# Performance work log

Measured on AMD Instinct MI355X. Metric: run time of the kernel, lower is better.

The kernel has to match this reference:

```python
import jax, jax.numpy as jnp
import numpy as np

B, T, C = 8, 1024, 1024
H, HS = 16, 64            # n_head, head_size
K, STRIDE = 32, 16        # block_length, stride_length
WIN = 128                 # local_window_size
EPS = 1e-5


def _ln(z, w):
    m = jnp.mean(z, axis=-1, keepdims=True)
    v = jnp.var(z, axis=-1, keepdims=True)
    return (z - m) / jnp.sqrt(v + EPS) * w


def setup_inputs() -> dict:
    key = jax.random.key(0)
    ks = jax.random.split(key, 8)
    s = 0.02
    return {
        "x": jax.random.normal(ks[0], (B, T, C), jnp.float32),
        "c_attn_w": jax.random.normal(ks[1], (3 * C, C), jnp.float32) * s,
        "conv_w": jax.random.normal(ks[2], (HS, HS, K), jnp.float32) * s,
        "ln_comp_w": jnp.ones((HS,), jnp.float32),
        "ln_local_w": jnp.ones((C,), jnp.float32),
        "gate_w1": jax.random.normal(ks[3], (C, 2 * C), jnp.float32) * s,
        "gate_ln_w": jnp.ones((C,), jnp.float32),
        "gate_w2": jax.random.normal(ks[4], (2, C), jnp.float32) * s,
        "c_proj_w": jax.random.normal(ks[5], (C, C), jnp.float32) * s,
    }


def reference(x, c_attn_w, conv_w, ln_comp_w, ln_local_w, gate_w1, gate_ln_w, gate_w2, c_proj_w):
    qkv = jnp.einsum('btc,oc->bto', x, c_attn_w)          # [B,T,3C]
    q, k, v = jnp.split(qkv, 3, axis=-1)
    def heads(t):
        return t.reshape(B, T, H, HS).transpose(0, 2, 1, 3)  # [B,H,T,hs]
    q, k, v = heads(q), heads(k), heads(v)

    # CompressionMLP: Conv1d over time + LayerNorm(hs) + exact GELU
    def compress(t):
        xr = t.transpose(0, 1, 3, 2).reshape(B * H, HS, T)   # [B*H, hs, T]
        co = jax.lax.conv_general_dilated(
            xr, conv_w, window_strides=(STRIDE,), padding='VALID',
            dimension_numbers=('NCH', 'OIH', 'NCH'))          # [B*H, hs, NB]
        co = co.transpose(0, 2, 1)                            # [B*H, NB, hs]
        co = jax.nn.gelu(_ln(co, ln_comp_w), approximate=False)
        nb = co.shape[1]
        return co.reshape(B, H, nb, HS)

    kc = compress(k)
    vc = compress(v)
    NB = kc.shape[2]  # 63
    scale = 1.0 / np.sqrt(HS)

    ti = jnp.arange(T)
    band = (ti[None, :] <= ti[:, None]) & (ti[None, :] >= ti[:, None] - WIN)  # [T,T]
    s_loc = jnp.einsum('bhqd,bhkd->bhqk', q, k) * scale
    s_loc = jnp.where(band[None, None], s_loc, -jnp.inf)
    local_out = jnp.einsum('bhqk,bhkd->bhqd', jax.nn.softmax(s_loc, axis=-1), v)
    local_out = local_out.transpose(0, 2, 1, 3).reshape(B, T, C)
    local_norm = _ln(local_out, ln_local_w)

    # compressed-KV attention with block-causal mask: block j <= token i
    bj = jnp.arange(NB)
    cmask = bj[None, :] <= ti[:, None]                        # [T,NB]
    s_cmp = jnp.einsum('bhqd,bhkd->bhqk', q, kc) * scale
    s_cmp = jnp.where(cmask[None, None], s_cmp, -jnp.inf)
    comp_out = jnp.einsum('bhqk,bhkd->bhqd', jax.nn.softmax(s_cmp, axis=-1), vc)
    comp_out = comp_out.transpose(0, 2, 1, 3).reshape(B, T, C)

    # AttentionGating: last-token features -> Linear -> LN -> ReLU -> Linear -> softmax
    feats = jnp.concatenate([local_norm[:, -1, :], comp_out[:, -1, :]], axis=-1)  # [B,2C]
    h = jax.nn.relu(_ln(feats @ gate_w1.T, gate_ln_w))
    gates = jax.nn.softmax(h @ gate_w2.T, axis=-1)            # [B,2]

    combined = gates[:, None, 0:1] * local_norm + gates[:, None, 1:2] * comp_out
    y = jnp.einsum('btc,oc->bto', combined, c_proj_w)
    return y
```

## Files before the change

### kernel.cpp

```cpp
#include <hip/hip_runtime.h>
#include <cstdint>
#include <cmath>
#include <cstddef>

typedef unsigned int u32;
typedef unsigned short u16;
typedef __bf16 bf16x8 __attribute__((ext_vector_type(8)));
typedef float f32x4 __attribute__((ext_vector_type(4)));
typedef u32 u32x4 __attribute__((ext_vector_type(4)));
typedef u32 u32x2 __attribute__((ext_vector_type(2)));

#define DEV static __device__ __forceinline__

DEV float bflo(u32 u) { return __uint_as_float(u << 16); }
DEV float bfhi(u32 u) { return __uint_as_float(u & 0xffff0000u); }
DEV u16 f2bf(float f) {
  u32 u = __float_as_uint(f);
  u += 0x7fffu + ((u >> 16) & 1u);
  return (u16)(u >> 16);
}
DEV f32x4 unpack_bf4(u32x2 r) {
  return (f32x4){bflo(r[0]), bfhi(r[0]), bflo(r[1]), bfhi(r[1])};
}
DEV float wredsum(float v) {
#pragma unroll
  for (int o = 32; o; o >>= 1) v += __shfl_xor(v, o, 64);
  return v;
}

DEV void gload_lds16(const u16* g, u16* lds_base) {
  __builtin_amdgcn_global_load_lds((const __attribute__((address_space(1))) void*)g,
                                   (__attribute__((address_space(3))) void*)lds_base,
                                   16, 0, 0);
}

__global__ __launch_bounds__(256) void fused_cast(const float* __restrict__ x,
                                                  const float* __restrict__ aw,
                                                  const float* __restrict__ pw,
                                                  const float* __restrict__ cw,
                                                  u16* __restrict__ xb,
                                                  u16* __restrict__ wab,
                                                  u16* __restrict__ wpb,
                                                  u16* __restrict__ wcb,
                                                  u16* __restrict__ kcb,
                                                  u16* __restrict__ vcb) {
  const int blk = blockIdx.x;
  if (blk < 12288) {
    const float* src;
    u16* dst;
    int base;
    if (blk < 8192) { src = x; dst = xb; base = blk; }
    else if (blk < 11264) { src = aw; dst = wab; base = blk - 8192; }
    else { src = pw; dst = wpb; base = blk - 11264; }
    const size_t idx = ((size_t)base * 256 + threadIdx.x) * 4;
    const f32x4 v = *(const f32x4*)&src[idx];
    u32x2 r;
    r[0] = (u32)f2bf(v[0]) | ((u32)f2bf(v[1]) << 16);
    r[1] = (u32)f2bf(v[2]) | ((u32)f2bf(v[3]) << 16);
    *(u32x2*)&dst[idx] = r;
  } else if (blk < 12800) {
    const int idx = (blk - 12288) * 256 + threadIdx.x;
    const int o = idx >> 11;
    const int rest = idx & 2047;
    const int i = rest >> 5;
    const int kk = rest & 31;
    wcb[(o << 11) + (kk << 6) + i] = f2bf(cw[idx]);
  } else {
    for (int i = threadIdx.x; i < 8192; i += 256) {
      const int bh = i >> 6, d = i & 63;
      kcb[bh * 4096 + 63 * 64 + d] = 0;
      vcb[bh * 4096 + d * 64 + 63] = 0;
    }
  }
}

template <int OUT_BF16>
__global__ __launch_bounds__(256, 4) void gemm_bt(const u16* __restrict__ A,
                                                  const u16* __restrict__ Bm,
                                                  void* __restrict__ out,
                                                  int M, int N, int K) {
  __shared__ u16 As[128 * 32];
  __shared__ u16 Bs[128 * 32];
  const int tid = threadIdx.x;
  const int lane = tid & 63;
  const int w = tid >> 6;
  const int row0 = blockIdx.x * 128;
  const int col0 = blockIdx.y * 128;
  const int wm = (w >> 1) * 64, wn = (w & 1) * 64;
  const int lr = lane & 15, lq = lane >> 4;
  const int srow = lane >> 2;
  const int scol = (lane & 3) * 8;

  f32x4 acc[4][4] = {};

  for (int k0 = 0; k0 < K; k0 += 32) {
    __syncthreads();
#pragma unroll
    for (int p = 0; p < 2; ++p) {
      const int base_r = p * 64 + w * 16;
      gload_lds16(&A[(size_t)(row0 + base_r + srow) * K + k0 + scol], &As[base_r * 32]);
      gload_lds16(&Bm[(size_t)(col0 + base_r + srow) * K + k0 + scol], &Bs[base_r * 32]);
    }
    __syncthreads();
    bf16x8 af[4], bfr[4];
#pragma unroll
    for (int i = 0; i < 4; ++i) {
      af[i] = *(const bf16x8*)&As[(wm + i * 16 + lr) * 32 + lq * 8];
      bfr[i] = *(const bf16x8*)&Bs[(wn + i * 16 + lr) * 32 + lq * 8];
    }
#pragma unroll
    for (int i = 0; i < 4; ++i)
#pragma unroll
      for (int j = 0; j < 4; ++j)
        acc[i][j] = __builtin_amdgcn_mfma_f32_16x16x32_bf16(af[i], bfr[j], acc[i][j], 0, 0, 0);
  }
#pragma unroll
  for (int i = 0; i < 4; ++i)
#pragma unroll
    for (int j = 0; j < 4; ++j)
#pragma unroll
      for (int rr = 0; rr < 4; ++rr) {
        const int gr = row0 + wm + i * 16 + lq * 4 + rr;
        const int gc = col0 + wn + j * 16 + lr;
        const float v = acc[i][j][rr];
        if (OUT_BF16)
          ((u16*)out)[(size_t)gr * N + gc] = f2bf(v);
        else
          ((float*)out)[(size_t)gr * N + gc] = v;
      }
}

__global__ __launch_bounds__(256) void compress_kernel(const u16* __restrict__ qkv,
                                                       const u16* __restrict__ Wc,
                                                       const float* __restrict__ ln_w,
                                                       u16* __restrict__ kcb,
                                                       u16* __restrict__ vcb) {
  __shared__ u16 As[2][64 * 32];
  __shared__ u16 Bs[2][64 * 32];
  __shared__ float Cs[64][65];
  const int tid = threadIdx.x;
  const int lane = tid & 63, w = tid >> 6;
  const int lr = lane & 15, lq = lane >> 4;
  const int r0 = blockIdx.x * 64;
  const int srcoff = 1024 + (int)blockIdx.y * 1024;

  const int arow = tid >> 2, acol = (tid & 3) * 8;
  const int gr = r0 + arow;
  const int bh = gr / 63;
  const int nb = gr - bh * 63;
  const int b = bh >> 4, h = bh & 15;
  const size_t abase = (size_t)(b * 1024 + nb * 16) * 3072 + srcoff + h * 64 + acol;
  const size_t bbase = (size_t)arow * 2048 + acol;

  f32x4 acc[4] = {};
  {
    gload_lds16(&qkv[abase], &As[0][w * 512]);
    gload_lds16(&Wc[bbase], &Bs[0][w * 512]);
  }
  for (int it = 0; it < 64; ++it) {
    const int cur = it & 1;
    __syncthreads();
    if (it < 63) {
      const int k0 = (it + 1) * 32;
      const int kk = k0 >> 6, i0 = k0 & 63;
      gload_lds16(&qkv[abase + (size_t)kk * 3072 + i0], &As[cur ^ 1][w * 512]);
      gload_lds16(&Wc[bbase + k0], &Bs[cur ^ 1][w * 512]);
    }
    const bf16x8 af = *(const bf16x8*)&As[cur][(w * 16 + lr) * 32 + lq * 8];
#pragma unroll
    for (int j = 0; j < 4; ++j) {
      const bf16x8 bfr = *(const bf16x8*)&Bs[cur][(j * 16 + lr) * 32 + lq * 8];
      acc[j] = __builtin_amdgcn_mfma_f32_16x16x32_bf16(af, bfr, acc[j], 0, 0, 0);
    }
  }
  __syncthreads();
#pragma unroll
  for (int j = 0; j < 4; ++j)
#pragma unroll
    for (int rr = 0; rr < 4; ++rr)
      Cs[w * 16 + lq * 4 + rr][j * 16 + lr] = acc[j][rr];
  __syncthreads();
  if (tid < 64) {
    const int gr2 = r0 + tid;
    const int bh2 = gr2 / 63;
    const int nb2 = gr2 - bh2 * 63;
    float s = 0.f, s2 = 0.f;
#pragma unroll 8
    for (int d = 0; d < 64; ++d) {
      const float xv = Cs[tid][d];
      s += xv;
      s2 += xv * xv;
    }
    const float m = s * (1.f / 64.f);
    const float inv = rsqrtf(s2 * (1.f / 64.f) - m * m + 1e-5f);
    if (blockIdx.y == 0) {
      const size_t gb = (size_t)bh2 * 4096 + nb2 * 64;
#pragma unroll 8
      for (int d = 0; d < 64; ++d) {
        const float z = (Cs[tid][d] - m) * inv * ln_w[d];
        kcb[gb + d] = f2bf(0.5f * z * (1.f + erff(z * 0.70710678118f)));
      }
    } else {
      const size_t gb = (size_t)bh2 * 4096 + nb2;
#pragma unroll 8
      for (int d = 0; d < 64; ++d) {
        const float z = (Cs[tid][d] - m) * inv * ln_w[d];
        vcb[gb + d * 64] = f2bf(0.5f * z * (1.f + erff(z * 0.70710678118f)));
      }
    }
  }
}

__global__ __launch_bounds__(256) void attn_fused(const u16* __restrict__ qkv,
                                                  const u16* __restrict__ kcb,
                                                  const u16* __restrict__ vcb,
                                                  u16* __restrict__ loc,
                                                  u16* __restrict__ outc) {
  __shared__ __align__(16) char smem[53248];
  u16* Ks = (u16*)smem;
  u16* Vt = (u16*)smem;
  u16* Ps = (u16*)(smem + 27648);
  const int bh = blockIdx.x;
  const int b = bh >> 4, h = bh & 15;
  const int i0 = blockIdx.y * 64;
  const int jbase = i0 - 128;
  const int tid = threadIdx.x;
  const int lane = tid & 63, w = tid >> 6;
  const int lr = lane & 15, lq = lane >> 4;

  u32x4 vreg[6];
#pragma unroll
  for (int c = 0; c < 6; ++c) {
    const int lin = c * 256 + tid;
    const int s = lin >> 3, d0 = (lin & 7) * 8;
    const int j = jbase + s;
    u32x4 kval = {0, 0, 0, 0}, vval = {0, 0, 0, 0};
    if (j >= 0) {
      const size_t ro = (size_t)(b * 1024 + j) * 3072 + h * 64 + d0;
      kval = *(const u32x4*)&qkv[ro + 1024];
      vval = *(const u32x4*)&qkv[ro + 2048];
    }
    vreg[c] = vval;
    *(u32x4*)&Ks[s * 72 + d0] = kval;
  }
  bf16x8 qf[2];
  {
    const size_t qrow = (size_t)(b * 1024 + i0 + w * 16 + lr) * 3072 + h * 64;
#pragma unroll
    for (int ks = 0; ks < 2; ++ks) qf[ks] = *(const bf16x8*)&qkv[qrow + ks * 32 + lq * 8];
  }
  __syncthreads();

  f32x4 sa[9];
#pragma unroll
  for (int j9 = 0; j9 < 9; ++j9) sa[j9] = (f32x4){0.f, 0.f, 0.f, 0.f};
#pragma unroll
  for (int ks = 0; ks < 2; ++ks)
#pragma unroll
    for (int j9 = 0; j9 < 9; ++j9) {
      const int jt = w + j9;
      const bf16x8 kf = *(const bf16x8*)&Ks[(jt * 16 + lr) * 72 + ks * 32 + lq * 8];
      sa[j9] = __builtin_amdgcn_mfma_f32_16x16x32_bf16(qf[ks], kf, sa[j9], 0, 0, 0);
    }

  const float NINF = -__builtin_inff();
  float mx[4] = {NINF, NINF, NINF, NINF};
#pragma unroll
  for (int j9 = 0; j9 < 9; ++j9) {
    const int s = (w + j9) * 16 + lr;
#pragma unroll
    for (int rr = 0; rr < 4; ++rr) {
      const int qi = w * 16 + lq * 4 + rr;
      const bool valid = (jbase + s >= 0) && (s >= qi) && (s <= qi + 128);
      const float v = valid ? sa[j9][rr] * 0.125f : NINF;
      sa[j9][rr] = v;
      mx[rr] = fmaxf(mx[rr], v);
    }
  }
#pragma unroll
  for (int rr = 0; rr < 4; ++rr)
#pragma unroll
    for (int o = 1; o < 16; o <<= 1) mx[rr] = fmaxf(mx[rr], __shfl_xor(mx[rr], o, 64));
  float sum[4] = {0.f, 0.f, 0.f, 0.f};
#pragma unroll
  for (int j9 = 0; j9 < 9; ++j9)
#pragma unroll
    for (int rr = 0; rr < 4; ++rr) {
      const float p = __expf(sa[j9][rr] - mx[rr]);
      sa[j9][rr] = p;
      sum[rr] += p;
    }
#pragma unroll
  for (int rr = 0; rr < 4; ++rr) {
#pragma unroll
    for (int o = 1; o < 16; o <<= 1) sum[rr] += __shfl_xor(sum[rr], o, 64);
    sum[rr] = 1.0f / sum[rr];
  }
  __syncthreads();

#pragma unroll
  for (int j9 = 0; j9 < 9; ++j9) {
    const int jt = w + j9;
#pragma unroll
    for (int rr = 0; rr < 4; ++rr)
      Ps[(w * 16 + lq * 4 + rr) * 200 + jt * 16 + lr] = f2bf(sa[j9][rr] * sum[rr]);
  }
  {
    const int jz = (w == 0) ? 9 : (w == 1) ? 0 : (w == 2) ? 11 : 2;
#pragma unroll
    for (int rr = 0; rr < 4; ++rr) Ps[(w * 16 + lq * 4 + rr) * 200 + jz * 16 + lr] = 0;
  }
#pragma unroll
  for (int c = 0; c < 6; ++c) {
    const int lin = c * 256 + tid;
    const int s = lin >> 3, d0 = (lin & 7) * 8;
    const u32x4 val = vreg[c];
#pragma unroll
    for (int q = 0; q < 4; ++q) {
      Vt[(d0 + 2 * q) * 200 + s] = (u16)(val[q] & 0xffffu);
      Vt[(d0 + 2 * q + 1) * 200 + s] = (u16)(val[q] >> 16);
    }
  }
  __syncthreads();

  const int W = (w >> 1) * 32;
  f32x4 oa[4];
#pragma unroll
  for (int jt = 0; jt < 4; ++jt) oa[jt] = (f32x4){0.f, 0.f, 0.f, 0.f};
#pragma unroll
  for (int ks = 0; ks < 5; ++ks) {
    const bf16x8 pf = *(const bf16x8*)&Ps[(w * 16 + lr) * 200 + W + ks * 32 + lq * 8];
#pragma unroll
    for (int jt = 0; jt < 4; ++jt) {
      const bf16x8 vf = *(const bf16x8*)&Vt[(jt * 16 + lr) * 200 + W + ks * 32 + lq * 8];
      oa[jt] = __builtin_amdgcn_mfma_f32_16x16x32_bf16(pf, vf, oa[jt], 0, 0, 0);
    }
  }
#pragma unroll
  for (int jt = 0; jt < 4; ++jt)
#pragma unroll
    for (int rr = 0; rr < 4; ++rr)
      loc[(size_t)(b * 1024 + i0 + w * 16 + lq * 4 + rr) * 1024 + h * 64 + jt * 16 + lr] =
          f2bf(oa[jt][rr]);

  __syncthreads();
  u16* Kc = (u16*)smem;
  u16* Vc = (u16*)(smem + 9216);
  u16* Pc = (u16*)(smem + 18432);
  const size_t cb = (size_t)bh * 4096;
  for (int c2 = tid; c2 < 512; c2 += 256) {
    const int nb = c2 >> 3, d0 = (c2 & 7) * 8;
    *(u32x4*)&Kc[nb * 72 + d0] = *(const u32x4*)&kcb[cb + nb * 64 + d0];
  }
  for (int c2 = tid; c2 < 512; c2 += 256) {
    const int d = c2 >> 3, n0 = (c2 & 7) * 8;
    *(u32x4*)&Vc[d * 72 + n0] = *(const u32x4*)&vcb[cb + d * 64 + n0];
  }
  __syncthreads();

  f32x4 ca[4];
#pragma unroll
  for (int j = 0; j < 4; ++j) ca[j] = (f32x4){0.f, 0.f, 0.f, 0.f};
#pragma unroll
  for (int ks = 0; ks < 2; ++ks)
#pragma unroll
    for (int j = 0; j < 4; ++j) {
      const bf16x8 kf = *(const bf16x8*)&Kc[(j * 16 + lr) * 72 + ks * 32 + lq * 8];
      ca[j] = __builtin_amdgcn_mfma_f32_16x16x32_bf16(qf[ks], kf, ca[j], 0, 0, 0);
    }
  float mc[4] = {NINF, NINF, NINF, NINF};
#pragma unroll
  for (int j = 0; j < 4; ++j) {
    const int s = j * 16 + lr;
#pragma unroll
    for (int rr = 0; rr < 4; ++rr) {
      const int i = i0 + w * 16 + lq * 4 + rr;
      const bool valid = (s <= i) && (s < 63);
      const float v = valid ? ca[j][rr] * 0.125f : NINF;
      ca[j][rr] = v;
      mc[rr] = fmaxf(mc[rr], v);
    }
  }
#pragma unroll
  for (int rr = 0; rr < 4; ++rr)
#pragma unroll
    for (int o = 1; o < 16; o <<= 1) mc[rr] = fmaxf(mc[rr], __shfl_xor(mc[rr], o, 64));
  float sc[4] = {0.f, 0.f, 0.f, 0.f};
#pragma unroll
  for (int j = 0; j < 4; ++j)
#pragma unroll
    for (int rr = 0; rr < 4; ++rr) {
      const float p = __expf(ca[j][rr] - mc[rr]);
      ca[j][rr] = p;
      sc[rr] += p;
    }
#pragma unroll
  for (int rr = 0; rr < 4; ++rr) {
#pragma unroll
    for (int o = 1; o < 16; o <<= 1) sc[rr] += __shfl_xor(sc[rr], o, 64);
    sc[rr] = 1.0f / sc[rr];
  }
#pragma unroll
  for (int j = 0; j < 4; ++j)
#pragma unroll
    for (int rr = 0; rr < 4; ++rr)
      Pc[(w * 16 + lq * 4 + rr) * 72 + j * 16 + lr] = f2bf(ca[j][rr] * sc[rr]);
  __syncthreads();

  f32x4 co[4];
#pragma unroll
  for (int jt = 0; jt < 4; ++jt) co[jt] = (f32x4){0.f, 0.f, 0.f, 0.f};
#pragma unroll
  for (int ks = 0; ks < 2; ++ks) {
    const bf16x8 pf = *(const bf16x8*)&Pc[(w * 16 + lr) * 72 + ks * 32 + lq * 8];
#pragma unroll
    for (int jt = 0; jt < 4; ++jt) {
      const bf16x8 vf = *(const bf16x8*)&Vc[(jt * 16 + lr) * 72 + ks * 32 + lq * 8];
      co[jt] = __builtin_amdgcn_mfma_f32_16x16x32_bf16(pf, vf, co[jt], 0, 0, 0);
    }
  }
#pragma unroll
  for (int jt = 0; jt < 4; ++jt)
#pragma unroll
    for (int rr = 0; rr < 4; ++rr)
      outc[(size_t)(b * 1024 + i0 + w * 16 + lq * 4 + rr) * 1024 + h * 64 + jt * 16 + lr] =
          f2bf(co[jt][rr]);
}

__global__ __launch_bounds__(256) void ln_feats(const u16* __restrict__ locb,
                                                const u16* __restrict__ compb,
                                                const float* __restrict__ lnw,
                                                float* __restrict__ feats) {
  const int b = blockIdx.x, tid = threadIdx.x;
  const size_t base = ((size_t)b * 1024 + 1023) * 1024 + tid * 4;
  const f32x4 v = unpack_bf4(*(const u32x2*)&locb[base]);
  float s = v[0] + v[1] + v[2] + v[3];
  float s2 = v[0] * v[0] + v[1] * v[1] + v[2] * v[2] + v[3] * v[3];
  s = wredsum(s);
  s2 = wredsum(s2);
  __shared__ float rs[4], rs2[4];
  const int w = tid >> 6, lane = tid & 63;
  if (!lane) { rs[w] = s; rs2[w] = s2; }
  __syncthreads();
  s = rs[0] + rs[1] + rs[2] + rs[3];
  s2 = rs2[0] + rs2[1] + rs2[2] + rs2[3];
  const float m = s * (1.f / 1024.f);
  const float inv = rsqrtf(s2 * (1.f / 1024.f) - m * m + 1e-5f);
  const f32x4 wv = *(const f32x4*)&lnw[tid * 4];
  f32x4 o;
#pragma unroll
  for (int k = 0; k < 4; ++k) o[k] = (v[k] - m) * inv * wv[k];
  *(f32x4*)&feats[b * 2048 + tid * 4] = o;
  *(f32x4*)&feats[b * 2048 + 1024 + tid * 4] = unpack_bf4(*(const u32x2*)&compb[base]);
}

__global__ __launch_bounds__(256) void gate_gemv(const float* __restrict__ feats,
                                                 const float* __restrict__ w1,
                                                 float* __restrict__ hraw) {
  const int o = blockIdx.x * 4 + (threadIdx.x >> 6);
  const int lane = threadIdx.x & 63;
  const float* wr = &w1[(size_t)o * 2048];
  float acc[8] = {};
#pragma unroll
  for (int it = 0; it < 8; ++it) {
    const int c = (it * 64 + lane) * 4;
    const f32x4 wv = *(const f32x4*)&wr[c];
#pragma unroll
    for (int b = 0; b < 8; ++b) {
      const f32x4 fv = *(const f32x4*)&feats[b * 2048 + c];
      acc[b] += fv[0] * wv[0] + fv[1] * wv[1] + fv[2] * wv[2] + fv[3] * wv[3];
    }
  }
#pragma unroll
  for (int b = 0; b < 8; ++b) acc[b] = wredsum(acc[b]);
  if (lane == 0) {
#pragma unroll
    for (int b = 0; b < 8; ++b) hraw[b * 1024 + o] = acc[b];
  }
}

__global__ __launch_bounds__(256) void gate_fin(const float* __restrict__ hraw,
                                                const float* __restrict__ lnw,
                                                const float* __restrict__ w2,
                                                float* __restrict__ gates) {
  const int b = blockIdx.x, tid = threadIdx.x;
  const f32x4 v = *(const f32x4*)&hraw[(size_t)b * 1024 + tid * 4];
  float s = v[0] + v[1] + v[2] + v[3];
  float s2 = v[0] * v[0] + v[1] * v[1] + v[2] * v[2] + v[3] * v[3];
  s = wredsum(s);
  s2 = wredsum(s2);
  __shared__ float rs[4], rs2[4];
  const int w = tid >> 6, lane = tid & 63;
  if (!lane) { rs[w] = s; rs2[w] = s2; }
  __syncthreads();
  s = rs[0] + rs[1] + rs[2] + rs[3];
  s2 = rs2[0] + rs2[1] + rs2[2] + rs2[3];
  const float m = s * (1.f / 1024.f);
  const float inv = rsqrtf(s2 * (1.f / 1024.f) - m * m + 1e-5f);
  float p0 = 0.f, p1 = 0.f;
#pragma unroll
  for (int k = 0; k < 4; ++k) {
    float hh = (v[k] - m) * inv * lnw[tid * 4 + k];
    hh = fmaxf(hh, 0.f);
    p0 += hh * w2[tid * 4 + k];
    p1 += hh * w2[1024 + tid * 4 + k];
  }
  p0 = wredsum(p0);
  p1 = wredsum(p1);
  __syncthreads();
  if (!lane) { rs[w] = p0; rs2[w] = p1; }
  __syncthreads();
  if (tid == 0) {
    const float l0 = rs[0] + rs[1] + rs[2] + rs[3];
    const float l1 = rs2[0] + rs2[1] + rs2[2] + rs2[3];
    const float mm = fmaxf(l0, l1);
    const float e0 = __expf(l0 - mm), e1 = __expf(l1 - mm);
    const float iv = 1.f / (e0 + e1);
    gates[b * 2] = e0 * iv;
    gates[b * 2 + 1] = e1 * iv;
  }
}

__global__ __launch_bounds__(256) void combine_ln_cast(const u16* __restrict__ locb,
                                                       const u16* __restrict__ compb,
                                                       const float* __restrict__ lnw,
                                                       const float* __restrict__ gates,
                                                       u16* __restrict__ outb) {
  const int row = blockIdx.x, tid = threadIdx.x;
  const size_t base = (size_t)row * 1024 + tid * 4;
  const f32x4 v = unpack_bf4(*(const u32x2*)&locb[base]);
  float s = v[0] + v[1] + v[2] + v[3];
  float s2 = v[0] * v[0] + v[1] * v[1] + v[2] * v[2] + v[3] * v[3];
  s = wredsum(s);
  s2 = wredsum(s2);
  __shared__ float rs[4], rs2[4];
  const int w = tid >> 6, lane = tid & 63;
  if (!lane) { rs[w] = s; rs2[w] = s2; }
  __syncthreads();
  s = rs[0] + rs[1] + rs[2] + rs[3];
  s2 = rs2[0] + rs2[1] + rs2[2] + rs2[3];
  const float m = s * (1.f / 1024.f);
  const float inv = rsqrtf(s2 * (1.f / 1024.f) - m * m + 1e-5f);
  const int b = row >> 10;
  const float g0 = gates[2 * b], g1 = gates[2 * b + 1];
  const f32x4 wv = *(const f32x4*)&lnw[tid * 4];
  const f32x4 c = unpack_bf4(*(const u32x2*)&compb[base]);
  float ov[4];
#pragma unroll
  for (int k = 0; k < 4; ++k) ov[k] = g0 * ((v[k] - m) * inv * wv[k]) + g1 * c[k];
  u32x2 r;
  r[0] = (u32)f2bf(ov[0]) | ((u32)f2bf(ov[1]) << 16);
  r[1] = (u32)f2bf(ov[2]) | ((u32)f2bf(ov[3]) << 16);
  *(u32x2*)&outb[base] = r;
}

extern "C" void kernel_launch(void* const* d_in, const int* in_sizes, int n_in,
                              void* d_out, int out_size, void* d_ws, size_t ws_size,
                              hipStream_t stream) {
  const float* x = (const float*)d_in[0];
  const float* c_attn_w = (const float*)d_in[1];
  const float* conv_w = (const float*)d_in[2];
  const float* ln_comp_w = (const float*)d_in[3];
  const float* ln_local_w = (const float*)d_in[4];
  const float* gate_w1 = (const float*)d_in[5];
  const float* gate_ln_w = (const float*)d_in[6];
  const float* gate_w2 = (const float*)d_in[7];
  const float* c_proj_w = (const float*)d_in[8];
  float* y = (float*)d_out;

  char* ws = (char*)d_ws;
  size_t off = 0;
  auto alloc = [&](size_t bytes) -> void* {
    void* p = ws + off;
    off += (bytes + 255) & ~(size_t)255;
    return p;
  };
  u16* qkvb = (u16*)alloc((size_t)8192 * 3072 * 2);
  u16* xb = (u16*)alloc((size_t)8192 * 1024 * 2);
  u16* wab = (u16*)alloc((size_t)3072 * 1024 * 2);
  u16* wpb = (u16*)alloc((size_t)1024 * 1024 * 2);
  u16* wcb = (u16*)alloc((size_t)64 * 2048 * 2);
  u16* kcb = (u16*)alloc((size_t)128 * 4096 * 2);
  u16* vcb = (u16*)alloc((size_t)128 * 4096 * 2);
  u16* locb = (u16*)alloc((size_t)8192 * 1024 * 2);
  u16* compb = (u16*)alloc((size_t)8192 * 1024 * 2);
  float* feats = (float*)alloc((size_t)8 * 2048 * 4);
  float* hraw = (float*)alloc((size_t)8192 * 4);
  float* gates = (float*)alloc(64);
  u16* combb = (u16*)alloc((size_t)8192 * 1024 * 2);

  fused_cast<<<12801, 256, 0, stream>>>(x, c_attn_w, c_proj_w, conv_w, xb, wab, wpb, wcb, kcb,
                                        vcb);

  gemm_bt<1><<<dim3(64, 24), 256, 0, stream>>>(xb, wab, qkvb, 8192, 3072, 1024);

  compress_kernel<<<dim3(126, 2), 256, 0, stream>>>(qkvb, wcb, ln_comp_w, kcb, vcb);

  attn_fused<<<dim3(128, 16), 256, 0, stream>>>(qkvb, kcb, vcb, locb, compb);

  ln_feats<<<8, 256, 0, stream>>>(locb, compb, ln_local_w, feats);
  gate_gemv<<<256, 256, 0, stream>>>(feats, gate_w1, hraw);
  gate_fin<<<8, 256, 0, stream>>>(hraw, gate_ln_w, gate_w2, gates);

  combine_ln_cast<<<8192, 256, 0, stream>>>(locb, compb, ln_local_w, gates, combb);

  gemm_bt<0><<<dim3(64, 8), 256, 0, stream>>>(combb, wpb, y, 8192, 1024, 1024);
}
```

Baseline: 300.1 us.

## Deepen GEMM K-tile with swizzled LDS and halve compress tile rows

The bf16 GEMM now stages 64-wide K slices instead of 32, halving the number of barrier-separated iterations. It also adds an XOR swizzle on LDS columns to avoid bank conflicts on fragment reads. Separately, the compression conv kernel uses 32-row tiles with waves split across rows and columns, doubling the grid to 504 blocks so more CUs stay busy. Costs are more LDS per GEMM block, which may reduce occupancy, and more redundant weight loads in the compression kernel.

```diff
diff --git a/kernel.cpp b/kernel.cpp
--- a/kernel.cpp
+++ b/kernel.cpp
@@ -79,8 +79,8 @@
                                                   const u16* __restrict__ Bm,
                                                   void* __restrict__ out,
                                                   int M, int N, int K) {
-  __shared__ u16 As[128 * 32];
-  __shared__ u16 Bs[128 * 32];
+  __shared__ u16 As[128 * 64];
+  __shared__ u16 Bs[128 * 64];
   const int tid = threadIdx.x;
   const int lane = tid & 63;
   const int w = tid >> 6;
@@ -88,31 +88,36 @@
   const int col0 = blockIdx.y * 128;
   const int wm = (w >> 1) * 64, wn = (w & 1) * 64;
   const int lr = lane & 15, lq = lane >> 4;
-  const int srow = lane >> 2;
-  const int scol = (lane & 3) * 8;
+  const int srow = lane >> 3;
+  const int scol = ((lane & 7) ^ (srow & 7)) * 8;
+  const int pgA = ((lq ^ (lr & 7)) * 8);
 
   f32x4 acc[4][4] = {};
 
-  for (int k0 = 0; k0 < K; k0 += 32) {
+  for (int k0 = 0; k0 < K; k0 += 64) {
     __syncthreads();
 #pragma unroll
-    for (int p = 0; p < 2; ++p) {
-      const int base_r = p * 64 + w * 16;
-      gload_lds16(&A[(size_t)(row0 + base_r + srow) * K + k0 + scol], &As[base_r * 32]);
-      gload_lds16(&Bm[(size_t)(col0 + base_r + srow) * K + k0 + scol], &Bs[base_r * 32]);
+    for (int c = 0; c < 4; ++c) {
+      const int base_r = w * 32 + c * 8;
+      gload_lds16(&A[(size_t)(row0 + base_r + srow) * K + k0 + scol], &As[base_r * 64]);
+      gload_lds16(&Bm[(size_t)(col0 + base_r + srow) * K + k0 + scol], &Bs[base_r * 64]);
     }
     __syncthreads();
-    bf16x8 af[4], bfr[4];
-#pragma unroll
-    for (int i = 0; i < 4; ++i) {
-      af[i] = *(const bf16x8*)&As[(wm + i * 16 + lr) * 32 + lq * 8];
-      bfr[i] = *(const bf16x8*)&Bs[(wn + i * 16 + lr) * 32 + lq * 8];
-    }
-#pragma unroll
-    for (int i = 0; i < 4; ++i)
-#pragma unroll
-      for (int j = 0; j < 4; ++j)
-        acc[i][j] = __builtin_amdgcn_mfma_f32_16x16x32_bf16(af[i], bfr[j], acc[i][j], 0, 0, 0);
+#pragma unroll
+    for (int ks = 0; ks < 2; ++ks) {
+      const int pg = pgA ^ (ks << 5);
+      bf16x8 af[4], bfr[4];
+#pragma unroll
+      for (int i = 0; i < 4; ++i) {
+        af[i] = *(const bf16x8*)&As[(wm + i * 16 + lr) * 64 + pg];
+        bfr[i] = *(const bf16x8*)&Bs[(wn + i * 16 + lr) * 64 + pg];
+      }
+#pragma unroll
+      for (int i = 0; i < 4; ++i)
+#pragma unroll
+        for (int j = 0; j < 4; ++j)
+          acc[i][j] = __builtin_amdgcn_mfma_f32_16x16x32_bf16(af[i], bfr[j], acc[i][j], 0, 0, 0);
+    }
   }
 #pragma unroll
   for (int i = 0; i < 4; ++i)
@@ -135,52 +140,55 @@
                                                        const float* __restrict__ ln_w,
                                                        u16* __restrict__ kcb,
                                                        u16* __restrict__ vcb) {
-  __shared__ u16 As[2][64 * 32];
+  __shared__ u16 As[2][32 * 32];
   __shared__ u16 Bs[2][64 * 32];
-  __shared__ float Cs[64][65];
+  __shared__ float Cs[32][65];
   const int tid = threadIdx.x;
   const int lane = tid & 63, w = tid >> 6;
   const int lr = lane & 15, lq = lane >> 4;
-  const int r0 = blockIdx.x * 64;
+  const int r0 = blockIdx.x * 32;
   const int srcoff = 1024 + (int)blockIdx.y * 1024;
 
-  const int arow = tid >> 2, acol = (tid & 3) * 8;
-  const int gr = r0 + arow;
-  const int bh = gr / 63;
-  const int nb = gr - bh * 63;
-  const int b = bh >> 4, h = bh & 15;
-  const size_t abase = (size_t)(b * 1024 + nb * 16) * 3072 + srcoff + h * 64 + acol;
-  const size_t bbase = (size_t)arow * 2048 + acol;
-
-  f32x4 acc[4] = {};
-  {
-    gload_lds16(&qkv[abase], &As[0][w * 512]);
-    gload_lds16(&Wc[bbase], &Bs[0][w * 512]);
-  }
+  const int srow = lane >> 2, scol = (lane & 3) * 8;
+  const size_t bbase = (size_t)(w * 16 + srow) * 2048 + scol;
+  size_t abase = 0;
+  if (w < 2) {
+    const int gr = r0 + w * 16 + srow;
+    const int bh = gr / 63;
+    const int nb = gr - bh * 63;
+    const int b = bh >> 4, h = bh & 15;
+    abase = (size_t)(b * 1024 + nb * 16) * 3072 + srcoff + h * 64 + scol;
+  }
+  const int rw = (w & 1) * 16;
+  const int cw = (w >> 1) * 32;
+
+  f32x4 acc[2] = {};
+  gload_lds16(&Wc[bbase], &Bs[0][w * 512]);
+  if (w < 2) gload_lds16(&qkv[abase], &As[0][w * 512]);
   for (int it = 0; it < 64; ++it) {
     const int cur = it & 1;
     __syncthreads();
     if (it < 63) {
       const int k0 = (it + 1) * 32;
       const int kk = k0 >> 6, i0 = k0 & 63;
-      gload_lds16(&qkv[abase + (size_t)kk * 3072 + i0], &As[cur ^ 1][w * 512]);
       gload_lds16(&Wc[bbase + k0], &Bs[cur ^ 1][w * 512]);
-    }
-    const bf16x8 af = *(const bf16x8*)&As[cur][(w * 16 + lr) * 32 + lq * 8];
-#pragma unroll
-    for (int j = 0; j < 4; ++j) {
-      const bf16x8 bfr = *(const bf16x8*)&Bs[cur][(j * 16 + lr) * 32 + lq * 8];
+      if (w < 2) gload_lds16(&qkv[abase + (size_t)kk * 3072 + i0], &As[cur ^ 1][w * 512]);
+    }
+    const bf16x8 af = *(const bf16x8*)&As[cur][(rw + lr) * 32 + lq * 8];
+#pragma unroll
+    for (int j = 0; j < 2; ++j) {
+      const bf16x8 bfr = *(const bf16x8*)&Bs[cur][(cw + j * 16 + lr) * 32 + lq * 8];
       acc[j] = __builtin_amdgcn_mfma_f32_16x16x32_bf16(af, bfr, acc[j], 0, 0, 0);
     }
   }
   __syncthreads();
 #pragma unroll
-  for (int j = 0; j < 4; ++j)
+  for (int j = 0; j < 2; ++j)
 #pragma unroll
     for (int rr = 0; rr < 4; ++rr)
-      Cs[w * 16 + lq * 4 + rr][j * 16 + lr] = acc[j][rr];
-  __syncthreads();
-  if (tid < 64) {
+      Cs[rw + lq * 4 + rr][cw + j * 16 + lr] = acc[j][rr];
+  __syncthreads();
+  if (tid < 32) {
     const int gr2 = r0 + tid;
     const int bh2 = gr2 / 63;
     const int nb2 = gr2 - bh2 * 63;
@@ -594,7 +602,7 @@
 
   gemm_bt<1><<<dim3(64, 24), 256, 0, stream>>>(xb, wab, qkvb, 8192, 3072, 1024);
 
-  compress_kernel<<<dim3(126, 2), 256, 0, stream>>>(qkvb, wcb, ln_comp_w, kcb, vcb);
+  compress_kernel<<<dim3(252, 2), 256, 0, stream>>>(qkvb, wcb, ln_comp_w, kcb, vcb);
 
   attn_fused<<<dim3(128, 16), 256, 0, stream>>>(qkvb, kcb, vcb, locb, compb);
 
```

New measurement: 280.2 us. 6.6% less time.
